# Performance work log

Measured on AMD Instinct MI355X. Metric: run time of the kernel, lower is better.

## Reference

```python
import jax, jax.numpy as jnp
import numpy as np

# snntorch default ATan surrogate (alpha=2): fwd = heaviside, bwd = g / (1 + (pi*x)^2)
@jax.custom_vjp
def atan_spike(x):
    return (x > 0).astype(x.dtype)

def _atan_fwd(x):
    return atan_spike(x), x

def _atan_bwd(x, g):
    return (g / (1.0 + (jnp.pi * x) ** 2),)

atan_spike.defvjp(_atan_fwd, _atan_bwd)

B = 4096  # batch
D = 100   # row length / fc1 in-features; also number of timesteps (rows)
O = 3     # fc1 out-features

def setup_inputs() -> dict:
    key = jax.random.key(0)
    k1, k2, k3, k4 = jax.random.split(key, 4)
    x = jax.random.uniform(k1, (B, D, D), jnp.float32)   # rate-coding probabilities
    u = jax.random.uniform(k2, (B, D, D), jnp.float32)   # Bernoulli uniforms for rate coding
    lim = 1.0 / np.sqrt(D)
    W = jax.random.uniform(k3, (O, D), jnp.float32, -lim, lim)
    b = jax.random.uniform(k4, (O,), jnp.float32, -lim, lim)
    beta = jnp.float32(0.95)
    threshold = jnp.float32(1.0)
    return {"x": x, "u": u, "W": W, "b": b, "beta": beta, "threshold": threshold}

def reference(x, u, W, b, beta, threshold):
    # sgen.rate(x, 1)[0]: one-step Bernoulli rate coding, prob = x
    spikes = (u < x).astype(x.dtype)            # [B, 100, 100]
    seq = jnp.transpose(spikes, (1, 0, 2))      # [T=100, B, 100] (loop over rows)

    def step(mem, inp):                          # mem: [B, 3], inp: [B, 100]
        cur = inp @ W.T + b                      # fc1
        # snntorch Leaky, reset_mechanism='subtract': reset from previous mem, detached
        reset = jax.lax.stop_gradient(atan_spike(mem - threshold))
        mem = beta * mem + cur - reset * threshold
        spk = atan_spike(mem - threshold)
        return mem, (spk, mem)

    mem0 = jnp.zeros((x.shape[0], O), x.dtype)   # init_leaky()
    _, (spk_rec, mem_rec) = jax.lax.scan(step, mem0, seq)
    return spk_rec, mem_rec                      # each [100, B, 3]
```

## Files before the change

### kernel.cpp

```cpp
#include <hip/hip_runtime.h>

#define NB 4096
#define ND 100
#define NT 100
#define NO 3

__global__ __launch_bounds__(320) void fused_leaky(
    const float* __restrict__ x, const float* __restrict__ u,
    const float* __restrict__ W, const float* __restrict__ bias,
    const float* __restrict__ beta_p, const float* __restrict__ thr_p,
    float* __restrict__ out)
{
    __shared__ float cur_s[NT * 4];

    const int b   = blockIdx.x;
    const int tid = threadIdx.x;
    const int hw  = tid >> 5;
    const int l   = tid & 31;

    float4 w0 = {0,0,0,0}, w1 = {0,0,0,0}, w2 = {0,0,0,0};
    if (l < 25) {
        w0 = ((const float4*)(W         ))[l];
        w1 = ((const float4*)(W +    ND))[l];
        w2 = ((const float4*)(W + 2*ND ))[l];
    }

    const float* xb = x + (size_t)b * (ND * ND);
    const float* ub = u + (size_t)b * (ND * ND);

    for (int iter = 0; iter < 10; ++iter) {
        const int t = hw + 10 * iter;
        float a0 = 0.f, a1 = 0.f, a2 = 0.f;
        if (l < 25) {
            const float4 xv = ((const float4*)(xb + t * ND))[l];
            const float4 uv = ((const float4*)(ub + t * ND))[l];
            const float s0 = (uv.x < xv.x) ? 1.f : 0.f;
            const float s1 = (uv.y < xv.y) ? 1.f : 0.f;
            const float s2 = (uv.z < xv.z) ? 1.f : 0.f;
            const float s3 = (uv.w < xv.w) ? 1.f : 0.f;
            a0 = fmaf(s3, w0.w, fmaf(s2, w0.z, fmaf(s1, w0.y, s0 * w0.x)));
            a1 = fmaf(s3, w1.w, fmaf(s2, w1.z, fmaf(s1, w1.y, s0 * w1.x)));
            a2 = fmaf(s3, w2.w, fmaf(s2, w2.z, fmaf(s1, w2.y, s0 * w2.x)));
        }
        #pragma unroll
        for (int m = 1; m < 32; m <<= 1) {
            a0 += __shfl_xor(a0, m);
            a1 += __shfl_xor(a1, m);
            a2 += __shfl_xor(a2, m);
        }
        if (l == 0) {
            cur_s[t * 4 + 0] = a0;
            cur_s[t * 4 + 1] = a1;
            cur_s[t * 4 + 2] = a2;
        }
    }
    __syncthreads();

    if (tid < NO) {
        const int   o    = tid;
        const float beta = beta_p[0];
        const float thr  = thr_p[0];
        const float bo   = bias[o];
        const int   col  = b * NO + o;
        float* mem_rec = out + (size_t)NT * NB * NO;

        float mem = 0.f;
        #pragma unroll 4
        for (int t = 0; t < NT; ++t) {
            const float cv   = cur_s[t * 4 + o] + bo;
            const float rsub = (mem > thr) ? thr : 0.f;
            mem = __fadd_rn(__fadd_rn(__fmul_rn(beta, mem), cv), -rsub);
            const float s = (mem > thr) ? 1.f : 0.f;
            out[(size_t)t * (NB * NO) + col]     = s;
            mem_rec[(size_t)t * (NB * NO) + col] = mem;
        }
    }
}

extern "C" void kernel_launch(void* const* d_in, const int* in_sizes, int n_in,
                              void* d_out, int out_size, void* d_ws, size_t ws_size,
                              hipStream_t stream) {
    const float* x    = (const float*)d_in[0];
    const float* u    = (const float*)d_in[1];
    const float* W    = (const float*)d_in[2];
    const float* bias = (const float*)d_in[3];
    const float* beta = (const float*)d_in[4];
    const float* thr  = (const float*)d_in[5];
    float* out = (float*)d_out;

    fused_leaky<<<NB, 320, 0, stream>>>(x, u, W, bias, beta, thr, out);
}
```

Before: 355.2 us.

## Assign one thread per timestep row and drop warp-shuffle reductions

Each block now uses 128 threads, and each thread computes the full 100-element dot product for one row sequentially. Previously half-warps each handled one row and reduced partial sums with shuffles. Weights are staged in shared memory, and the current buffer is transposed to a per-output pitch layout. This removes the shuffle reduction and the idle lanes, but each thread now strides 400 bytes across rows, so global loads within a wavefront are uncoalesced. The data also requires more loop iterations per thread.

```diff
diff --git a/kernel.cpp b/kernel.cpp
--- a/kernel.cpp
+++ b/kernel.cpp
@@ -4,55 +4,47 @@
 #define ND 100
 #define NT 100
 #define NO 3
+#define CPITCH 101
 
-__global__ __launch_bounds__(320) void fused_leaky(
+__global__ __launch_bounds__(128) void fused_leaky(
     const float* __restrict__ x, const float* __restrict__ u,
     const float* __restrict__ W, const float* __restrict__ bias,
     const float* __restrict__ beta_p, const float* __restrict__ thr_p,
     float* __restrict__ out)
 {
-    __shared__ float cur_s[NT * 4];
+    __shared__ float Ws[25][NO][4];
+    __shared__ float cur_s[NO][CPITCH];
 
     const int b   = blockIdx.x;
     const int tid = threadIdx.x;
-    const int hw  = tid >> 5;
-    const int l   = tid & 31;
 
-    float4 w0 = {0,0,0,0}, w1 = {0,0,0,0}, w2 = {0,0,0,0};
-    if (l < 25) {
-        w0 = ((const float4*)(W         ))[l];
-        w1 = ((const float4*)(W +    ND))[l];
-        w2 = ((const float4*)(W + 2*ND ))[l];
+    if (tid < 75) {
+        const int o = tid / 25;
+        const int p = tid - o * 25;
+        const float4 w = ((const float4*)(W + o * ND))[p];
+        Ws[p][o][0] = w.x; Ws[p][o][1] = w.y; Ws[p][o][2] = w.z; Ws[p][o][3] = w.w;
     }
+    __syncthreads();
 
-    const float* xb = x + (size_t)b * (ND * ND);
-    const float* ub = u + (size_t)b * (ND * ND);
-
-    for (int iter = 0; iter < 10; ++iter) {
-        const int t = hw + 10 * iter;
+    if (tid < NT) {
+        const float4* xr = (const float4*)(x + (size_t)b * (ND * ND) + tid * ND);
+        const float4* ur = (const float4*)(u + (size_t)b * (ND * ND) + tid * ND);
         float a0 = 0.f, a1 = 0.f, a2 = 0.f;
-        if (l < 25) {
-            const float4 xv = ((const float4*)(xb + t * ND))[l];
-            const float4 uv = ((const float4*)(ub + t * ND))[l];
+        #pragma unroll 5
+        for (int p = 0; p < 25; ++p) {
+            const float4 xv = xr[p];
+            const float4 uv = ur[p];
             const float s0 = (uv.x < xv.x) ? 1.f : 0.f;
             const float s1 = (uv.y < xv.y) ? 1.f : 0.f;
             const float s2 = (uv.z < xv.z) ? 1.f : 0.f;
             const float s3 = (uv.w < xv.w) ? 1.f : 0.f;
-            a0 = fmaf(s3, w0.w, fmaf(s2, w0.z, fmaf(s1, w0.y, s0 * w0.x)));
-            a1 = fmaf(s3, w1.w, fmaf(s2, w1.z, fmaf(s1, w1.y, s0 * w1.x)));
-            a2 = fmaf(s3, w2.w, fmaf(s2, w2.z, fmaf(s1, w2.y, s0 * w2.x)));
+            a0 = fmaf(s3, Ws[p][0][3], fmaf(s2, Ws[p][0][2], fmaf(s1, Ws[p][0][1], fmaf(s0, Ws[p][0][0], a0))));
+            a1 = fmaf(s3, Ws[p][1][3], fmaf(s2, Ws[p][1][2], fmaf(s1, Ws[p][1][1], fmaf(s0, Ws[p][1][0], a1))));
+            a2 = fmaf(s3, Ws[p][2][3], fmaf(s2, Ws[p][2][2], fmaf(s1, Ws[p][2][1], fmaf(s0, Ws[p][2][0], a2))));
         }
-        #pragma unroll
-        for (int m = 1; m < 32; m <<= 1) {
-            a0 += __shfl_xor(a0, m);
-            a1 += __shfl_xor(a1, m);
-            a2 += __shfl_xor(a2, m);
-        }
-        if (l == 0) {
-            cur_s[t * 4 + 0] = a0;
-            cur_s[t * 4 + 1] = a1;
-            cur_s[t * 4 + 2] = a2;
-        }
+        cur_s[0][tid] = a0;
+        cur_s[1][tid] = a1;
+        cur_s[2][tid] = a2;
     }
     __syncthreads();
 
@@ -67,7 +59,7 @@
         float mem = 0.f;
         #pragma unroll 4
         for (int t = 0; t < NT; ++t) {
-            const float cv   = cur_s[t * 4 + o] + bo;
+            const float cv   = cur_s[o][t] + bo;
             const float rsub = (mem > thr) ? thr : 0.f;
             mem = __fadd_rn(__fadd_rn(__fmul_rn(beta, mem), cv), -rsub);
             const float s = (mem > thr) ? 1.f : 0.f;
@@ -88,5 +80,5 @@
     const float* thr  = (const float*)d_in[5];
     float* out = (float*)d_out;
 
-    fused_leaky<<<NB, 320, 0, stream>>>(x, u, W, bias, beta, thr, out);
+    fused_leaky<<<NB, 128, 0, stream>>>(x, u, W, bias, beta, thr, out);
 }
```

After: 384.8 us. 1.08x slower.
